# Optimization experiments

Measured on AMD Instinct MI355X. Metric: run time of the kernel, lower is better.

Reference implementation:

```python
import math
import jax, jax.numpy as jnp
import numpy as np

D_MODEL = 256
NUM_HEAD = 8
NUM_LEVEL = 1
KERNEL = 5
NUM_POINT = KERNEL * KERNEL
NUM_VAR = 5  # with_rotation=True
HEAD_DIM = D_MODEL // NUM_HEAD


def _kernel_indices(k=KERNEL):
    # odd kernel: linspace(-(k-1)/2, (k-1)/2, k); torch.meshgrid default 'ij'; stack([j,i])/k
    idx = jnp.linspace(-(k - 1) / 2.0, (k - 1) / 2.0, k)
    ii, jj = jnp.meshgrid(idx, idx, indexing='ij')
    return jnp.stack([jj, ii], axis=-1).reshape(-1, 2) / k  # (P, 2)


def setup_inputs() -> dict:
    key = jax.random.key(0)
    ks = jax.random.split(key, 8)
    B, LQ = 2, 4096
    Hf, Wf = 188, 188
    LV = Hf * Wf
    d = D_MODEL
    nb = NUM_LEVEL * NUM_HEAD * NUM_VAR
    na = NUM_HEAD * NUM_LEVEL * NUM_POINT
    return {
        'query': jax.random.normal(ks[0], (B, LQ, d), jnp.float32),
        'value': jax.random.normal(ks[1], (B, LV, d), jnp.float32),
        'ref_windows': jax.random.uniform(ks[2], (B, LQ, 7), jnp.float32),
        'W_box': jax.random.normal(ks[3], (nb, d), jnp.float32) * 0.02,
        'b_box': jax.random.uniform(ks[4], (nb,), jnp.float32),
        'W_attn': jax.random.normal(ks[5], (na, d), jnp.float32) * 0.02,
        'b_attn': jnp.zeros((na,), jnp.float32),
        'W_value': jax.random.normal(ks[6], (d, d), jnp.float32) * 0.02,
        'b_value': jnp.zeros((d,), jnp.float32),
        'W_out': jax.random.normal(ks[7], (d, d), jnp.float32) * 0.02,
        'b_out': jnp.zeros((d,), jnp.float32),
        'H_feat': Hf,
        'W_feat': Wf,
    }


def reference(query, value, ref_windows, W_box, b_box, W_attn, b_attn,
              W_value, b_value, W_out, b_out, H_feat, W_feat):
    B, LQ, d = query.shape
    LV = value.shape[1]
    Hh, Lv, P, Dh = NUM_HEAD, NUM_LEVEL, NUM_POINT, HEAD_DIM

    # value projection -> (B, LV, Hh, Dh)
    v = (value @ W_value.T + b_value).reshape(B, LV, Hh, Dh)

    # attention weights: softmax over (level*point) per head
    attn = jax.nn.softmax((query @ W_attn.T + b_attn).reshape(B, LQ, Hh, Lv * P), axis=-1)
    attn = attn.reshape(B, LQ, Hh, Lv, P)

    # --- _where_to_attend ---
    ob = (query @ W_box.T + b_box).reshape(B, LQ, Hh, Lv, NUM_VAR)
    rw = ref_windows[:, :, None, None, :]                    # (B,LQ,1,1,7)
    ref_boxes = rw[..., jnp.array([0, 1, 3, 4])]             # cx, cy, w, h
    ref_angles = rw[..., 6:7]
    off_boxes, off_angles = ob[..., :4], ob[..., 4:5]
    angles = (ref_angles + off_angles / 16.0) * (2.0 * math.pi)
    boxes = ref_boxes + off_boxes / 8.0 * ref_boxes[..., jnp.array([2, 3, 2, 3])]
    center = boxes[..., None, :2]                            # (B,LQ,Hh,Lv,1,2)
    size = boxes[..., None, 2:4]
    cos_a, sin_a = jnp.cos(angles), jnp.sin(angles)
    rot = jnp.stack([cos_a, -sin_a, sin_a, cos_a], axis=-1).reshape(B, LQ, Hh, Lv, 1, 2, 2)
    g = _kernel_indices() * jax.nn.relu(size)                # (B,LQ,Hh,Lv,P,2)
    grid = center + (g[..., None, :] * rot).sum(-1)          # (B,LQ,Hh,Lv,P,2), normalized [0,1]

    # --- single-level bilinear sampling (align_corners=False, zero padding) ---
    gl = grid[:, :, :, 0]                                    # (B,LQ,Hh,P,2)
    gx = gl[..., 0] * W_feat - 0.5
    gy = gl[..., 1] * H_feat - 0.5
    x0 = jnp.floor(gx)
    y0 = jnp.floor(gy)
    x0i = x0.astype(jnp.int32)
    y0i = y0.astype(jnp.int32)
    wx1 = gx - x0
    wy1 = gy - y0
    wx0 = 1.0 - wx1
    wy0 = 1.0 - wy1

    b_idx = jnp.arange(B)[:, None, None, None]
    h_idx = jnp.arange(Hh)[None, None, :, None]

    def gather(yi, xi):
        valid = (xi >= 0) & (xi < W_feat) & (yi >= 0) & (yi < H_feat)
        lin = jnp.clip(yi, 0, H_feat - 1) * W_feat + jnp.clip(xi, 0, W_feat - 1)
        return v[b_idx, lin, h_idx] * valid[..., None]       # (B,LQ,Hh,P,Dh)

    s = (gather(y0i, x0i) * (wy0 * wx0)[..., None]
         + gather(y0i, x0i + 1) * (wy0 * wx1)[..., None]
         + gather(y0i + 1, x0i) * (wy1 * wx0)[..., None]
         + gather(y0i + 1, x0i + 1) * (wy1 * wx1)[..., None])

    out_heads = (s * attn[:, :, :, 0, :, None]).sum(axis=3)  # (B,LQ,Hh,Dh)
    out = out_heads.reshape(B, LQ, Hh * Dh) @ W_out.T + b_out
    attn_w = attn.reshape(B, LQ, Hh, Lv, KERNEL, KERNEL)
    return out, attn_w
```

## Files before the change

kernel.cpp:

```cpp
#include <hip/hip_runtime.h>


typedef float floatx4 __attribute__((ext_vector_type(4)));
typedef short shortx8 __attribute__((ext_vector_type(8)));

static __device__ __forceinline__ unsigned short f2bf(float x) {
    unsigned int u = __float_as_uint(x);
    return (unsigned short)((u + 0x7fffu + ((u >> 16) & 1u)) >> 16);
}
static __device__ __forceinline__ unsigned int pack2(float a, float b) {
    return (unsigned int)f2bf(a) | ((unsigned int)f2bf(b) << 16);
}
static __device__ __forceinline__ void async16(const void* g, void* lds) {
    __builtin_amdgcn_global_load_lds(
        (const __attribute__((address_space(1))) unsigned int*)g,
        (__attribute__((address_space(3))) unsigned int*)lds, 16, 0, 0);
}

__global__ __launch_bounds__(256) void convert_kernel(
    const float* __restrict__ value, unsigned short* __restrict__ vbf, long long nv4,
    const float* __restrict__ W_value, unsigned short* __restrict__ wvbf,
    const float* __restrict__ W_attn, const float* __restrict__ W_box,
    unsigned short* __restrict__ wabf, float* __restrict__ Wab,
    const float* __restrict__ W_out, unsigned short* __restrict__ wobf,
    const float* __restrict__ b_attn, const float* __restrict__ b_box,
    float* __restrict__ bab)
{
    const int NBV = 2048;
    const int blk = blockIdx.x, tid = threadIdx.x;
    if (blk < NBV) {
        for (long long i = (long long)blk * 256 + tid; i < nv4; i += (long long)NBV * 256) {
            float4 f = ((const float4*)value)[i];
            ((uint2*)vbf)[i] = make_uint2(pack2(f.x, f.y), pack2(f.z, f.w));
        }
    } else if (blk < NBV + 16) {
        int base = (blk - NBV) * 1024 + tid;
#pragma unroll
        for (int k = 0; k < 4; ++k) {
            int j = base + k * 256;
            float4 f = ((const float4*)W_value)[j];
            ((uint2*)wvbf)[j] = make_uint2(pack2(f.x, f.y), pack2(f.z, f.w));
        }
    } else if (blk < NBV + 32) {
        int base = (blk - NBV - 16) * 1024 + tid;
#pragma unroll
        for (int k = 0; k < 4; ++k) {
            int j = base + k * 256;
            int row = j >> 6, col = (j & 63) * 4;
            float4 f;
            if (row < 200)      f = *(const float4*)(W_attn + (size_t)row * 256 + col);
            else if (row < 240) f = *(const float4*)(W_box + (size_t)(row - 200) * 256 + col);
            else                f = make_float4(0.f, 0.f, 0.f, 0.f);
            ((uint2*)wabf)[j] = make_uint2(pack2(f.x, f.y), pack2(f.z, f.w));
            ((float4*)Wab)[j] = f;
        }
    } else if (blk < NBV + 48) {
        int base = (blk - NBV - 32) * 1024 + tid;
#pragma unroll
        for (int k = 0; k < 4; ++k) {
            int j = base + k * 256;
            float4 f = ((const float4*)W_out)[j];
            ((uint2*)wobf)[j] = make_uint2(pack2(f.x, f.y), pack2(f.z, f.w));
        }
    } else {
        bab[tid] = tid < 200 ? b_attn[tid] : (tid < 240 ? b_box[tid - 200] : 0.f);
    }
}

template <int OUTMODE>
__global__ __launch_bounds__(256) void gemm_bf16(
    const unsigned short* __restrict__ A,
    const unsigned short* __restrict__ Bw,
    const float* __restrict__ bias,
    void* __restrict__ Cv, int M, int LV)
{
    __shared__ unsigned short As[128 * 64];
    __shared__ unsigned short Bs[128 * 64];
    const int tid = threadIdx.x;
    const int wv = tid >> 6, lane = tid & 63;
    const int lr = lane & 15, lq = lane >> 4;
    const int m0 = blockIdx.x * 128, n0 = blockIdx.y * 128;
    const int wm = wv & 1, wn = wv >> 1;
    const int srow = tid >> 3;
    const int scol = (tid & 7) * 8;

    floatx4 acc[4][4];
#pragma unroll
    for (int i = 0; i < 4; ++i)
#pragma unroll
        for (int j = 0; j < 4; ++j) acc[i][j] = (floatx4){0.f, 0.f, 0.f, 0.f};

    for (int kc = 0; kc < 4; ++kc) {
        const int k0 = kc * 64;
        __syncthreads();
#pragma unroll
        for (int i = 0; i < 4; ++i) {
            int ra = m0 + i * 32 + srow; ra = ra < M ? ra : M - 1;
            async16(A + (size_t)ra * 256 + k0 + scol, (char*)As + i * 4096 + wv * 1024);
            int rb = n0 + i * 32 + srow;
            async16(Bw + (size_t)rb * 256 + k0 + scol, (char*)Bs + i * 4096 + wv * 1024);
        }
        __syncthreads();
#pragma unroll
        for (int kk = 0; kk < 64; kk += 32) {
            shortx8 af[4], bfr[4];
#pragma unroll
            for (int t = 0; t < 4; ++t) {
                af[t]  = *(const shortx8*)&As[(wm * 64 + t * 16 + lr) * 64 + kk + lq * 8];
                bfr[t] = *(const shortx8*)&Bs[(wn * 64 + t * 16 + lr) * 64 + kk + lq * 8];
            }
#pragma unroll
            for (int ti = 0; ti < 4; ++ti)
#pragma unroll
                for (int tj = 0; tj < 4; ++tj)
                    acc[ti][tj] = __builtin_amdgcn_mfma_f32_16x16x32_bf16(bfr[tj], af[ti], acc[ti][tj], 0, 0, 0);
        }
    }
#pragma unroll
    for (int ti = 0; ti < 4; ++ti) {
        int m = m0 + wm * 64 + ti * 16 + lr;
        if (m >= M) continue;
        if (OUTMODE == 0) {
            float* Crow = (float*)Cv + (size_t)m * 256;
#pragma unroll
            for (int tj = 0; tj < 4; ++tj) {
                int nb = n0 + wn * 64 + tj * 16 + lq * 4;
                float4 bv = *(const float4*)(bias + nb);
                float4 o = make_float4(acc[ti][tj][0] + bv.x, acc[ti][tj][1] + bv.y,
                                       acc[ti][tj][2] + bv.z, acc[ti][tj][3] + bv.w);
                *(float4*)(Crow + nb) = o;
            }
        } else {
            int b = m >= LV ? 1 : 0;
            int lv = m - (b ? LV : 0);
#pragma unroll
            for (int tj = 0; tj < 4; ++tj) {
                int nb = n0 + wn * 64 + tj * 16 + lq * 4;
                float4 bv = *(const float4*)(bias + nb);
                int h = nb >> 5, dh = nb & 31;
                unsigned short* dst = (unsigned short*)Cv + ((size_t)(b * 8 + h) * LV + lv) * 32 + dh;
                *(uint2*)dst = make_uint2(pack2(acc[ti][tj][0] + bv.x, acc[ti][tj][1] + bv.y),
                                          pack2(acc[ti][tj][2] + bv.z, acc[ti][tj][3] + bv.w));
            }
        }
    }
}

__global__ __launch_bounds__(256) void gemm_nt_bias(
    const float* __restrict__ A, const float* __restrict__ W,
    const float* __restrict__ bias, float* __restrict__ C, int M)
{
    const int K = 256, N = 256;
    __shared__ float As[16][68];
    __shared__ float Bs[16][68];
    int tid = threadIdx.x;
    int tcol = tid & 15, trow = tid >> 4;
    int m0 = blockIdx.x * 64, n0 = blockIdx.y * 64;
    int lr = tid >> 2, lc = (tid & 3) << 2;
    float acc[4][4] = {};
    for (int k0 = 0; k0 < K; k0 += 16) {
        int arow = m0 + lr; if (arow > M - 1) arow = M - 1;
        float4 av = *(const float4*)(A + (size_t)arow * K + k0 + lc);
        float4 wv = *(const float4*)(W + (size_t)(n0 + lr) * K + k0 + lc);
        __syncthreads();
        As[lc + 0][lr] = av.x; As[lc + 1][lr] = av.y; As[lc + 2][lr] = av.z; As[lc + 3][lr] = av.w;
        Bs[lc + 0][lr] = wv.x; Bs[lc + 1][lr] = wv.y; Bs[lc + 2][lr] = wv.z; Bs[lc + 3][lr] = wv.w;
        __syncthreads();
#pragma unroll
        for (int k = 0; k < 16; ++k) {
            float4 a4 = *(const float4*)&As[k][trow << 2];
            float4 b4 = *(const float4*)&Bs[k][tcol << 2];
            float a[4] = {a4.x, a4.y, a4.z, a4.w};
            float bb[4] = {b4.x, b4.y, b4.z, b4.w};
#pragma unroll
            for (int i = 0; i < 4; i++)
#pragma unroll
                for (int j = 0; j < 4; j++) acc[i][j] += a[i] * bb[j];
        }
    }
#pragma unroll
    for (int i = 0; i < 4; i++) {
        int m = m0 + trow * 4 + i;
        if (m >= M) continue;
#pragma unroll
        for (int j = 0; j < 4; j++) {
            int n = n0 + tcol * 4 + j;
            C[(size_t)m * N + n] = acc[i][j] + bias[n];
        }
    }
}

__global__ __launch_bounds__(256) void decode_sample_kernel(
    const unsigned short* __restrict__ v,
    const float* __restrict__ logits,
    const float* __restrict__ ref_windows,
    float* __restrict__ attn_out,
    unsigned short* __restrict__ ohbf,
    const int* __restrict__ Hf_p, const int* __restrict__ Wf_p, int LV, int LQ)
{
    __shared__ float lg[8][32];
    __shared__ float rw[8][7];
    __shared__ float prm[8][6];
    __shared__ float mxinv[8][2];
    __shared__ uint4 pk[8][25][2];

    const int s = blockIdx.x, c = blockIdx.y;
    const int b = s >> 3, h = s & 7;
    const int tid = threadIdx.x;
    const int Hf = *Hf_p, Wf = *Wf_p;
    const size_t mbase = (size_t)b * LQ + c * 8;

    if (tid < 240) {
        int qq = tid / 30, j = tid - qq * 30;
        int col = (j < 25) ? h * 25 + j : 200 + h * 5 + (j - 25);
        lg[qq][j] = logits[(mbase + qq) * 256 + col];
    }
    if (tid < 56) {
        int qq = tid / 7, k = tid - qq * 7;
        rw[qq][k] = ref_windows[(mbase + qq) * 7 + k];
    }
    __syncthreads();

    if (tid < 8) {
        int qq = tid;
        float mx = -1e30f;
#pragma unroll
        for (int p = 0; p < 25; p++) mx = fmaxf(mx, lg[qq][p]);
        float ssum = 0.f;
#pragma unroll
        for (int p = 0; p < 25; p++) ssum += expf(lg[qq][p] - mx);
        mxinv[qq][0] = mx; mxinv[qq][1] = 1.f / ssum;
        float cx = rw[qq][0] + lg[qq][25] * 0.125f * rw[qq][3];
        float cy = rw[qq][1] + lg[qq][26] * 0.125f * rw[qq][4];
        float bw = rw[qq][3] + lg[qq][27] * 0.125f * rw[qq][3];
        float bh = rw[qq][4] + lg[qq][28] * 0.125f * rw[qq][4];
        float ang = (rw[qq][6] + lg[qq][29] * 0.0625f) * 6.283185307179586f;
        prm[qq][0] = cx; prm[qq][1] = cy;
        prm[qq][2] = fmaxf(bw, 0.f); prm[qq][3] = fmaxf(bh, 0.f);
        prm[qq][4] = cosf(ang); prm[qq][5] = sinf(ang);
    }
    __syncthreads();

    if (tid < 200) {
        int qq = tid / 25, p = tid - qq * 25;
        float a = expf(lg[qq][p] - mxinv[qq][0]) * mxinv[qq][1];
        attn_out[(mbase + qq) * 200 + h * 25 + p] = a;
        int pi = p / 5, pj = p - pi * 5;
        float g0 = (float)(pj - 2) * 0.2f * prm[qq][2];
        float g1 = (float)(pi - 2) * 0.2f * prm[qq][3];
        float ca = prm[qq][4], sa = prm[qq][5];
        float gx = (prm[qq][0] + g0 * ca - g1 * sa) * (float)Wf - 0.5f;
        float gy = (prm[qq][1] + g0 * sa + g1 * ca) * (float)Hf - 0.5f;
        float x0f = floorf(gx), y0f = floorf(gy);
        int x0 = (int)x0f, y0 = (int)y0f;
        float wx1 = gx - x0f, wy1 = gy - y0f;
        float wx0 = 1.f - wx1, wy0 = 1.f - wy1;
        int y1 = y0 + 1;
        int bx; float wl, wr;
        if (x0 >= 0 && x0 <= Wf - 2)      { bx = x0;     wl = wx0; wr = wx1; }
        else if (x0 == -1)                { bx = 0;      wl = wx1; wr = 0.f; }
        else if (x0 == Wf - 1)            { bx = Wf - 2; wl = 0.f; wr = wx0; }
        else                              { bx = 0;      wl = 0.f; wr = 0.f; }
        float wy0v = (y0 >= 0 && y0 < Hf) ? wy0 : 0.f;
        float wy1v = (y1 >= 0 && y1 < Hf) ? wy1 : 0.f;
        int cy0 = min(max(y0, 0), Hf - 1), cy1 = min(max(y1, 0), Hf - 1);
        unsigned off0 = (unsigned)(cy0 * Wf + bx) * 16u;
        unsigned off1 = (unsigned)(cy1 * Wf + bx) * 16u;
        float aw0 = a * wy0v, aw1 = a * wy1v;
        pk[qq][p][0] = make_uint4(__float_as_uint(aw0 * wl), __float_as_uint(aw1 * wl), off0, off1);
        pk[qq][p][1] = make_uint4(__float_as_uint(aw0 * wr), __float_as_uint(aw1 * wr), off0, off1);
    }
    __syncthreads();

    const int qq = tid >> 5, l = tid & 31;
    const unsigned int* vw = (const unsigned int*)(v + (size_t)s * LV * 32);
    const uint4* pkp = &pk[qq][0][l >> 4];
    float e0 = 0.f, o0 = 0.f, e1 = 0.f, o1 = 0.f;
#pragma unroll
    for (int p = 0; p < 25; ++p) {
        uint4 t = pkp[2 * p];
        float w0 = __uint_as_float(t.x), w1 = __uint_as_float(t.y);
        unsigned u0 = vw[t.z + l];
        unsigned u1 = vw[t.w + l];
        e0 += w0 * __uint_as_float(u0 << 16);
        o0 += w0 * __uint_as_float(u0 & 0xffff0000u);
        e1 += w1 * __uint_as_float(u1 << 16);
        o1 += w1 * __uint_as_float(u1 & 0xffff0000u);
    }
    float a0 = e0 + e1, a1 = o0 + o1;
    a0 += __shfl_xor(a0, 16, 32);
    a1 += __shfl_xor(a1, 16, 32);
    if (l < 16)
        ((unsigned int*)ohbf)[(mbase + qq) * 128 + h * 16 + l] = pack2(a0, a1);
}

extern "C" void kernel_launch(void* const* d_in, const int* in_sizes, int n_in,
                              void* d_out, int out_size, void* d_ws, size_t ws_size,
                              hipStream_t stream) {
    const float* query       = (const float*)d_in[0];
    const float* value       = (const float*)d_in[1];
    const float* ref_windows = (const float*)d_in[2];
    const float* W_box       = (const float*)d_in[3];
    const float* b_box       = (const float*)d_in[4];
    const float* W_attn      = (const float*)d_in[5];
    const float* b_attn      = (const float*)d_in[6];
    const float* W_value     = (const float*)d_in[7];
    const float* b_value     = (const float*)d_in[8];
    const float* W_out       = (const float*)d_in[9];
    const float* b_out       = (const float*)d_in[10];
    const int*   Hf          = (const int*)d_in[11];
    const int*   Wf          = (const int*)d_in[12];

    const int M1 = in_sizes[1] / 256;
    const int MQ = in_sizes[0] / 256;
    const int LQ = MQ / 2;
    const int LV = M1 / 2;

    unsigned short* vbf  = (unsigned short*)d_ws;
    unsigned short* Vout = vbf + (size_t)M1 * 256;
    unsigned short* ohbf = Vout + (size_t)M1 * 256;
    unsigned short* wvbf = ohbf + (size_t)MQ * 256;
    unsigned short* wabf = wvbf + 65536;
    unsigned short* wobf = wabf + 65536;
    float* Wab       = (float*)(wobf + 65536);
    float* bab       = Wab + 65536;
    float* logits    = bab + 256;

    float* out0     = (float*)d_out;
    float* attn_out = out0 + (size_t)MQ * 256;

    const long long nv4 = (long long)M1 * 64;

    convert_kernel<<<2097, 256, 0, stream>>>(value, vbf, nv4, W_value, wvbf,
                                             W_attn, W_box, wabf, Wab,
                                             W_out, wobf, b_attn, b_box, bab);
    dim3 g1((M1 + 127) / 128, 2);
    gemm_bf16<1><<<g1, 256, 0, stream>>>(vbf, wvbf, b_value, Vout, M1, LV);
    dim3 g2(MQ / 64, 4);
    gemm_nt_bias<<<g2, 256, 0, stream>>>(query, Wab, bab, logits, MQ);
    decode_sample_kernel<<<dim3(16, LQ / 8), 256, 0, stream>>>(
        Vout, logits, ref_windows, attn_out, ohbf, Hf, Wf, LV, LQ);
    dim3 g4(MQ / 128, 2);
    gemm_bf16<0><<<g4, 256, 0, stream>>>(ohbf, wobf, b_out, out0, MQ, LV);
}
```

Baseline: 222.2 us.

## Fuse fp32-to-bf16 value conversion into GEMM and widen tiles to full N

Removes the separate pass that converted the large value tensor to bf16. The value GEMM now loads fp32 rows directly and converts them while staging into LDS. Blocks grow to 512 threads covering all 256 output columns, so each A tile is read once instead of twice. This drops one full write and read of the bf16 copy of value, but the A loads become synchronous register loads instead of async LDS loads, and each block needs more LDS.

```diff
diff --git a/kernel.cpp b/kernel.cpp
--- a/kernel.cpp
+++ b/kernel.cpp
@@ -17,8 +17,7 @@
         (__attribute__((address_space(3))) unsigned int*)lds, 16, 0, 0);
 }
 
-__global__ __launch_bounds__(256) void convert_kernel(
-    const float* __restrict__ value, unsigned short* __restrict__ vbf, long long nv4,
+__global__ __launch_bounds__(256) void convert_w(
     const float* __restrict__ W_value, unsigned short* __restrict__ wvbf,
     const float* __restrict__ W_attn, const float* __restrict__ W_box,
     unsigned short* __restrict__ wabf, float* __restrict__ Wab,
@@ -26,23 +25,17 @@
     const float* __restrict__ b_attn, const float* __restrict__ b_box,
     float* __restrict__ bab)
 {
-    const int NBV = 2048;
     const int blk = blockIdx.x, tid = threadIdx.x;
-    if (blk < NBV) {
-        for (long long i = (long long)blk * 256 + tid; i < nv4; i += (long long)NBV * 256) {
-            float4 f = ((const float4*)value)[i];
-            ((uint2*)vbf)[i] = make_uint2(pack2(f.x, f.y), pack2(f.z, f.w));
-        }
-    } else if (blk < NBV + 16) {
-        int base = (blk - NBV) * 1024 + tid;
+    if (blk < 16) {
+        int base = blk * 1024 + tid;
 #pragma unroll
         for (int k = 0; k < 4; ++k) {
             int j = base + k * 256;
             float4 f = ((const float4*)W_value)[j];
             ((uint2*)wvbf)[j] = make_uint2(pack2(f.x, f.y), pack2(f.z, f.w));
         }
-    } else if (blk < NBV + 32) {
-        int base = (blk - NBV - 16) * 1024 + tid;
+    } else if (blk < 32) {
+        int base = (blk - 16) * 1024 + tid;
 #pragma unroll
         for (int k = 0; k < 4; ++k) {
             int j = base + k * 256;
@@ -54,8 +47,8 @@
             ((uint2*)wabf)[j] = make_uint2(pack2(f.x, f.y), pack2(f.z, f.w));
             ((float4*)Wab)[j] = f;
         }
-    } else if (blk < NBV + 48) {
-        int base = (blk - NBV - 32) * 1024 + tid;
+    } else if (blk < 48) {
+        int base = (blk - 32) * 1024 + tid;
 #pragma unroll
         for (int k = 0; k < 4; ++k) {
             int j = base + k * 256;
@@ -67,22 +60,24 @@
     }
 }
 
-template <int OUTMODE>
-__global__ __launch_bounds__(256) void gemm_bf16(
-    const unsigned short* __restrict__ A,
+template <int OUTMODE, int AFP32>
+__global__ __launch_bounds__(512) void gemm_mfma(
+    const void* __restrict__ Av,
     const unsigned short* __restrict__ Bw,
     const float* __restrict__ bias,
     void* __restrict__ Cv, int M, int LV)
 {
     __shared__ unsigned short As[128 * 64];
-    __shared__ unsigned short Bs[128 * 64];
+    __shared__ unsigned short Bs[256 * 64];
     const int tid = threadIdx.x;
     const int wv = tid >> 6, lane = tid & 63;
     const int lr = lane & 15, lq = lane >> 4;
-    const int m0 = blockIdx.x * 128, n0 = blockIdx.y * 128;
     const int wm = wv & 1, wn = wv >> 1;
+    const int m0 = blockIdx.x * 128;
     const int srow = tid >> 3;
     const int scol = (tid & 7) * 8;
+    const int arow = tid >> 4;
+    const int acol4 = (tid & 15) * 4;
 
     floatx4 acc[4][4];
 #pragma unroll
@@ -95,10 +90,26 @@
         __syncthreads();
 #pragma unroll
         for (int i = 0; i < 4; ++i) {
-            int ra = m0 + i * 32 + srow; ra = ra < M ? ra : M - 1;
-            async16(A + (size_t)ra * 256 + k0 + scol, (char*)As + i * 4096 + wv * 1024);
-            int rb = n0 + i * 32 + srow;
-            async16(Bw + (size_t)rb * 256 + k0 + scol, (char*)Bs + i * 4096 + wv * 1024);
+            int rb = i * 64 + srow;
+            async16(Bw + (size_t)rb * 256 + k0 + scol, (char*)Bs + i * 8192 + wv * 1024);
+        }
+        if (AFP32) {
+            const float* A = (const float*)Av;
+#pragma unroll
+            for (int i = 0; i < 4; ++i) {
+                int rr = i * 32 + arow;
+                int gr = m0 + rr; gr = gr < M ? gr : M - 1;
+                float4 a = *(const float4*)(A + (size_t)gr * 256 + k0 + acol4);
+                *(uint2*)&As[rr * 64 + acol4] = make_uint2(pack2(a.x, a.y), pack2(a.z, a.w));
+            }
+        } else {
+            const unsigned short* A = (const unsigned short*)Av;
+#pragma unroll
+            for (int i = 0; i < 2; ++i) {
+                int rr = i * 64 + srow;
+                int gr = m0 + rr; gr = gr < M ? gr : M - 1;
+                async16(A + (size_t)gr * 256 + k0 + scol, (char*)As + i * 8192 + wv * 1024);
+            }
         }
         __syncthreads();
 #pragma unroll
@@ -124,18 +135,17 @@
             float* Crow = (float*)Cv + (size_t)m * 256;
 #pragma unroll
             for (int tj = 0; tj < 4; ++tj) {
-                int nb = n0 + wn * 64 + tj * 16 + lq * 4;
+                int nb = wn * 64 + tj * 16 + lq * 4;
                 float4 bv = *(const float4*)(bias + nb);
-                float4 o = make_float4(acc[ti][tj][0] + bv.x, acc[ti][tj][1] + bv.y,
-                                       acc[ti][tj][2] + bv.z, acc[ti][tj][3] + bv.w);
-                *(float4*)(Crow + nb) = o;
+                *(float4*)(Crow + nb) = make_float4(acc[ti][tj][0] + bv.x, acc[ti][tj][1] + bv.y,
+                                                    acc[ti][tj][2] + bv.z, acc[ti][tj][3] + bv.w);
             }
         } else {
             int b = m >= LV ? 1 : 0;
             int lv = m - (b ? LV : 0);
 #pragma unroll
             for (int tj = 0; tj < 4; ++tj) {
-                int nb = n0 + wn * 64 + tj * 16 + lq * 4;
+                int nb = wn * 64 + tj * 16 + lq * 4;
                 float4 bv = *(const float4*)(bias + nb);
                 int h = nb >> 5, dh = nb & 31;
                 unsigned short* dst = (unsigned short*)Cv + ((size_t)(b * 8 + h) * LV + lv) * 32 + dh;
@@ -316,8 +326,7 @@
     const int LQ = MQ / 2;
     const int LV = M1 / 2;
 
-    unsigned short* vbf  = (unsigned short*)d_ws;
-    unsigned short* Vout = vbf + (size_t)M1 * 256;
+    unsigned short* Vout = (unsigned short*)d_ws;
     unsigned short* ohbf = Vout + (size_t)M1 * 256;
     unsigned short* wvbf = ohbf + (size_t)MQ * 256;
     unsigned short* wabf = wvbf + 65536;
@@ -329,17 +338,12 @@
     float* out0     = (float*)d_out;
     float* attn_out = out0 + (size_t)MQ * 256;
 
-    const long long nv4 = (long long)M1 * 64;
-
-    convert_kernel<<<2097, 256, 0, stream>>>(value, vbf, nv4, W_value, wvbf,
-                                             W_attn, W_box, wabf, Wab,
-                                             W_out, wobf, b_attn, b_box, bab);
-    dim3 g1((M1 + 127) / 128, 2);
-    gemm_bf16<1><<<g1, 256, 0, stream>>>(vbf, wvbf, b_value, Vout, M1, LV);
+    convert_w<<<49, 256, 0, stream>>>(W_value, wvbf, W_attn, W_box, wabf, Wab,
+                                      W_out, wobf, b_attn, b_box, bab);
+    gemm_mfma<1, 1><<<(M1 + 127) / 128, 512, 0, stream>>>(value, wvbf, b_value, Vout, M1, LV);
     dim3 g2(MQ / 64, 4);
     gemm_nt_bias<<<g2, 256, 0, stream>>>(query, Wab, bab, logits, MQ);
     decode_sample_kernel<<<dim3(16, LQ / 8), 256, 0, stream>>>(
         Vout, logits, ref_windows, attn_out, ohbf, Hf, Wf, LV, LQ);
-    dim3 g4(MQ / 128, 2);
-    gemm_bf16<0><<<g4, 256, 0, stream>>>(ohbf, wobf, b_out, out0, MQ, LV);
-}
+    gemm_mfma<0, 0><<<MQ / 128, 512, 0, stream>>>(ohbf, wobf, b_out, out0, MQ, LV);
+}
```

Result: slower. 240.0 us (+8.0%).
